# Kernel tuning notes

Measured on AMD Instinct MI355X. Metric: run time of the kernel, lower is better.

The kernel has to match this reference:

```python
import jax, jax.numpy as jnp
import numpy as np

TAU = 1.0

def setup_inputs() -> dict:
    key = jax.random.key(0)
    scores = jax.random.normal(key, (16, 2048), dtype=jnp.float32)
    return {"scores": scores}

def reference(scores) -> jnp.ndarray:
    # scores: [B, n]
    B, n = scores.shape
    s = scores[:, :, None]                                  # [B, n, 1]
    # pairwise abs differences |s_i - s_j|
    A = jnp.abs(s - jnp.swapaxes(s, 1, 2))                  # [B, n, n]
    # torch: matmul(matmul(A, ones), ones^T) == row-sums broadcast over cols
    Bsum = jnp.sum(A, axis=-1, keepdims=True)               # [B, n, 1]
    # scaling_j = n + 1 - 2*(j+1)
    scaling = (n + 1 - 2 * (jnp.arange(n) + 1)).astype(scores.dtype)  # [n]
    C = s * scaling[None, None, :]                          # [B, n, n]
    P_max = jnp.swapaxes(C - Bsum, 1, 2)                    # [B, n, n]
    P_hat = jax.nn.softmax(P_max / TAU, axis=-1)
    return P_hat
```

## Files before the change

kernel.cpp:

```cpp
#include <hip/hip_runtime.h>
#include <math.h>

#define N 2048
#define BATCH 16

typedef float f32x4 __attribute__((ext_vector_type(4)));

__global__ __launch_bounds__(128) void bsum_kernel(const float* __restrict__ scores,
                                                   float* __restrict__ dsum) {
    __shared__ float s_sh[N];
    const int b = blockIdx.x >> 4;
    const int jBase = (blockIdx.x & 15) * 128;
    const float* s = scores + (size_t)b * N;

    for (int t = threadIdx.x; t < N / 4; t += 128) {
        ((float4*)s_sh)[t] = ((const float4*)s)[t];
    }
    __syncthreads();

    const int j = jBase + threadIdx.x;
    const float sj = s_sh[j];
    float acc = 0.f;
#pragma unroll 8
    for (int k = 0; k < N / 4; ++k) {
        float4 v = ((const float4*)s_sh)[k];
        acc += fabsf(sj - v.x) + fabsf(sj - v.y) + fabsf(sj - v.z) + fabsf(sj - v.w);
    }
    dsum[(size_t)b * N + j] = acc;
}

__global__ __launch_bounds__(256) void softmax_kernel(const float* __restrict__ scores,
                                                      const float* __restrict__ dsum,
                                                      float* __restrict__ out) {
    const int waveId = blockIdx.x * 4 + (threadIdx.x >> 6);
    const int lane = threadIdx.x & 63;
    const int rowBase = waveId * 4;
    const int b = rowBase >> 11;
    const int i0 = rowBase & 2047;

    const float4* s4p = (const float4*)(scores + (size_t)b * N);
    const float4* d4p = (const float4*)(dsum + (size_t)b * N);

    float4 s4[8], d4[8];
#pragma unroll
    for (int it = 0; it < 8; ++it) {
        s4[it] = s4p[it * 64 + lane];
        d4[it] = d4p[it * 64 + lane];
    }

#pragma unroll 1
    for (int r = 0; r < 4; ++r) {
        const int row = i0 + r;
        const float c = (float)(N - 1 - 2 * row);

        float lg[32];
        float m = -INFINITY;
#pragma unroll
        for (int it = 0; it < 8; ++it) {
            float l0 = fmaf(c, s4[it].x, -d4[it].x);
            float l1 = fmaf(c, s4[it].y, -d4[it].y);
            float l2 = fmaf(c, s4[it].z, -d4[it].z);
            float l3 = fmaf(c, s4[it].w, -d4[it].w);
            lg[it * 4 + 0] = l0;
            lg[it * 4 + 1] = l1;
            lg[it * 4 + 2] = l2;
            lg[it * 4 + 3] = l3;
            m = fmaxf(m, fmaxf(fmaxf(l0, l1), fmaxf(l2, l3)));
        }
#pragma unroll
        for (int off = 32; off > 0; off >>= 1)
            m = fmaxf(m, __shfl_xor(m, off, 64));

        float sum = 0.f;
#pragma unroll
        for (int k = 0; k < 32; ++k) {
            lg[k] = __expf(lg[k] - m);
            sum += lg[k];
        }
#pragma unroll
        for (int off = 32; off > 0; off >>= 1)
            sum += __shfl_xor(sum, off, 64);

        const float inv = 1.0f / sum;

        f32x4* orow = (f32x4*)(out + (((size_t)b * N) + row) * N);
#pragma unroll
        for (int it = 0; it < 8; ++it) {
            f32x4 o;
            o.x = lg[it * 4 + 0] * inv;
            o.y = lg[it * 4 + 1] * inv;
            o.z = lg[it * 4 + 2] * inv;
            o.w = lg[it * 4 + 3] * inv;
            __builtin_nontemporal_store(o, &orow[it * 64 + lane]);
        }
    }
}

extern "C" void kernel_launch(void* const* d_in, const int* in_sizes, int n_in,
                              void* d_out, int out_size, void* d_ws, size_t ws_size,
                              hipStream_t stream) {
    const float* scores = (const float*)d_in[0];
    float* out = (float*)d_out;
    float* dsum = (float*)d_ws;

    bsum_kernel<<<BATCH * 16, 128, 0, stream>>>(scores, dsum);
    softmax_kernel<<<32768 / 16, 256, 0, stream>>>(scores, dsum, out);
}
```

Measured before the change: 277.5 us.

## Split softmax into log-sum-exp stats kernel and massively parallel write kernel

The fused softmax kernel is replaced by two kernels. The first computes each row's max plus log-sum-exp and stores it to workspace. The second launches one block per half-row and writes exp(logit - lse) with plain vector stores. This aims to raise parallelism for the 256 MB output write, which was previously issued by few waves each handling four rows serially. In exchange it adds a launch, recomputes the exponentials, and drops the nontemporal store hint.

```diff
diff --git a/kernel.cpp b/kernel.cpp
--- a/kernel.cpp
+++ b/kernel.cpp
@@ -29,9 +29,9 @@
     dsum[(size_t)b * N + j] = acc;
 }
 
-__global__ __launch_bounds__(256) void softmax_kernel(const float* __restrict__ scores,
-                                                      const float* __restrict__ dsum,
-                                                      float* __restrict__ out) {
+__global__ __launch_bounds__(256) void stats_kernel(const float* __restrict__ scores,
+                                                    const float* __restrict__ dsum,
+                                                    float* __restrict__ qout) {
     const int waveId = blockIdx.x * 4 + (threadIdx.x >> 6);
     const int lane = threadIdx.x & 63;
     const int rowBase = waveId * 4;
@@ -61,10 +61,8 @@
             float l1 = fmaf(c, s4[it].y, -d4[it].y);
             float l2 = fmaf(c, s4[it].z, -d4[it].z);
             float l3 = fmaf(c, s4[it].w, -d4[it].w);
-            lg[it * 4 + 0] = l0;
-            lg[it * 4 + 1] = l1;
-            lg[it * 4 + 2] = l2;
-            lg[it * 4 + 3] = l3;
+            lg[it * 4 + 0] = l0; lg[it * 4 + 1] = l1;
+            lg[it * 4 + 2] = l2; lg[it * 4 + 3] = l3;
             m = fmaxf(m, fmaxf(fmaxf(l0, l1), fmaxf(l2, l3)));
         }
 #pragma unroll
@@ -73,27 +71,40 @@
 
         float sum = 0.f;
 #pragma unroll
-        for (int k = 0; k < 32; ++k) {
-            lg[k] = __expf(lg[k] - m);
-            sum += lg[k];
-        }
+        for (int k = 0; k < 32; ++k)
+            sum += __expf(lg[k] - m);
 #pragma unroll
         for (int off = 32; off > 0; off >>= 1)
             sum += __shfl_xor(sum, off, 64);
 
-        const float inv = 1.0f / sum;
+        if (lane == 0)
+            qout[rowBase + r] = m + __logf(sum);
+    }
+}
 
-        f32x4* orow = (f32x4*)(out + (((size_t)b * N) + row) * N);
-#pragma unroll
-        for (int it = 0; it < 8; ++it) {
-            f32x4 o;
-            o.x = lg[it * 4 + 0] * inv;
-            o.y = lg[it * 4 + 1] * inv;
-            o.z = lg[it * 4 + 2] * inv;
-            o.w = lg[it * 4 + 3] * inv;
-            __builtin_nontemporal_store(o, &orow[it * 64 + lane]);
-        }
-    }
+__global__ __launch_bounds__(256) void write_kernel(const float* __restrict__ scores,
+                                                    const float* __restrict__ dsum,
+                                                    const float* __restrict__ q,
+                                                    float* __restrict__ out) {
+    const int blk = blockIdx.x;
+    const int row = blk >> 1;
+    const int b = row >> 11;
+    const int i = row & 2047;
+    const int jBase = (blk & 1) * 1024 + threadIdx.x * 4;
+
+    const float c = (float)(N - 1 - 2 * i);
+    const float qv = q[row];
+
+    const float4 s4 = *(const float4*)(scores + (size_t)b * N + jBase);
+    const float4 B4 = *(const float4*)(dsum + (size_t)b * N + jBase);
+
+    f32x4 o;
+    o.x = __expf(fmaf(c, s4.x, -B4.x) - qv);
+    o.y = __expf(fmaf(c, s4.y, -B4.y) - qv);
+    o.z = __expf(fmaf(c, s4.z, -B4.z) - qv);
+    o.w = __expf(fmaf(c, s4.w, -B4.w) - qv);
+
+    *(f32x4*)(out + (size_t)row * N + jBase) = o;
 }
 
 extern "C" void kernel_launch(void* const* d_in, const int* in_sizes, int n_in,
@@ -102,7 +113,9 @@
     const float* scores = (const float*)d_in[0];
     float* out = (float*)d_out;
     float* dsum = (float*)d_ws;
+    float* q = (float*)d_ws + BATCH * N;
 
     bsum_kernel<<<BATCH * 16, 128, 0, stream>>>(scores, dsum);
-    softmax_kernel<<<32768 / 16, 256, 0, stream>>>(scores, dsum, out);
+    stats_kernel<<<BATCH * N / 16, 256, 0, stream>>>(scores, dsum, q);
+    write_kernel<<<BATCH * N * 2, 256, 0, stream>>>(scores, dsum, q, out);
 }
```

Measured after the change: 275.6 us. About the same (-0.7%).
